# Optimization experiments

Measured on AMD Instinct MI355X. Metric: run time of the kernel, lower is better.

## Reference

```python
import jax, jax.numpy as jnp
import numpy as np

B, K, C, L = 16, 8, 64, 2048
OFFSET = 2.0  # self.offset in Coupling
EPS = 1e-7    # clamp for logit stability (flows' safe_log analogue)


def setup_inputs() -> dict:
    key = jax.random.key(0)
    ks = jax.random.split(key, 6)
    return {
        "x_change": jax.random.normal(ks[0], (B, C, L), jnp.float32),
        "a": jax.random.normal(ks[1], (B, C, L), jnp.float32),
        "b": jax.random.normal(ks[2], (B, C, L), jnp.float32),
        "pi": jax.random.normal(ks[3], (B, K, C, L), jnp.float32),
        "mu": jax.random.normal(ks[4], (B, K, C, L), jnp.float32),
        "s": jax.random.normal(ks[5], (B, K, C, L), jnp.float32) * 0.1,  # log-scales
        "sldj": jnp.zeros((B,), jnp.float32),
    }


def reference(x_change, a, b, pi, mu, s, sldj):
    # scale = sigmoid(a + offset) + (1 - sigmoid(offset))
    sig_off = 1.0 - jax.nn.sigmoid(jnp.float32(OFFSET))
    scale = jax.nn.sigmoid(a + OFFSET) + sig_off                      # [B,C,L]

    logpi = jax.nn.log_softmax(pi, axis=1)                            # [B,K,C,L]
    z = (x_change[:, None] - mu) * jnp.exp(-s)                        # [B,K,C,L]

    # logistic.mixture_log_cdf: logsumexp_k(log pi_k + log sigmoid(z_k))
    log_cdf = jax.scipy.special.logsumexp(logpi + jax.nn.log_sigmoid(z), axis=1)
    u = jnp.clip(jnp.exp(log_cdf), EPS, 1.0 - EPS)                    # [B,C,L]

    # logistic.inverse (forward): logit, with ldj = -log(u) - log(1-u)
    y = jnp.log(u) - jnp.log1p(-u)
    scale_ldj = -jnp.log(u) - jnp.log1p(-u)

    # logistic.mixture_log_pdf: logsumexp_k(log pi_k + z - s - 2 softplus(z))
    log_pdf = jax.scipy.special.logsumexp(
        logpi + z - s - 2.0 * jax.nn.softplus(z), axis=1)             # [B,C,L]

    sldj_out = sldj + jnp.sum(
        (log_pdf + scale_ldj + jnp.log(scale)).reshape(sldj.shape[0], -1), axis=-1)
    out = (y + b) * scale                                             # [B,C,L]
    return out, sldj_out
```

## Files before the change

kernel.cpp:

```cpp
#include <hip/hip_runtime.h>

#define BB 16
#define KK 8
#define CC 64
#define LL 2048

constexpr int CL = CC * LL;
constexpr int QUADS_PER_BATCH = CL / 4;
constexpr int NBLOCKS = (BB * QUADS_PER_BATCH) / 256;

#define SIG_OFF 0.11920292202211755f
#define LOG_EPS -16.11809565095832f

#define DEPTH 4

typedef float f32x4 __attribute__((ext_vector_type(4)));

__device__ __forceinline__ float frcp(float x) { return __builtin_amdgcn_rcpf(x); }

__device__ __forceinline__ f32x4 ds_read128(uint32_t addr) {
    f32x4 r;
    asm volatile("ds_read_b128 %0, %1" : "=v"(r) : "v"(addr));
    return r;
}

__device__ __forceinline__ void glds16(const float* gsrc, const float* ldst) {
    __builtin_amdgcn_global_load_lds(
        (const __attribute__((address_space(1))) void*)gsrc,
        (__attribute__((address_space(3))) void*)ldst,
        16, 0, 0);
}

__global__ void init_sldj_kernel(const float* __restrict__ sldj_in,
                                 float* __restrict__ sldj_out) {
    int i = threadIdx.x;
    if (i < BB) sldj_out[i] = sldj_in[i];
}

__global__ __launch_bounds__(256) void coupling_kernel(
    const float* __restrict__ x,
    const float* __restrict__ a,
    const float* __restrict__ bv,
    const float* __restrict__ pi,
    const float* __restrict__ mu,
    const float* __restrict__ s,
    float* __restrict__ out,
    float* __restrict__ sldj_out) {

    __shared__ __align__(16) float lds[DEPTH][3][1024];

    const int tid = threadIdx.x;
    const int idx = blockIdx.x * 256 + tid;
    const int b   = idx >> 15;
    const int rem = idx & (QUADS_PER_BATCH - 1);
    const int base = b * CL + rem * 4;
    const int wid  = tid >> 6;

    const f32x4 x4 = *(const f32x4*)(x + base);
    const f32x4 a4 = *(const f32x4*)(a + base);
    const f32x4 b4 = *(const f32x4*)(bv + base);
    __builtin_amdgcn_sched_barrier(0);

    const int kb0 = (b * KK) * CL + rem * 4;
    const float* pik = pi + kb0;
    const float* muk = mu + kb0;
    const float* svk = s  + kb0;

#pragma unroll
    for (int k = 0; k < DEPTH; ++k) {
        glds16(pik + k * CL, &lds[k][0][wid * 256]);
        glds16(muk + k * CL, &lds[k][1][wid * 256]);
        glds16(svk + k * CL, &lds[k][2][wid * 256]);
    }
    __builtin_amdgcn_sched_barrier(0);

    auto* l3 = (__attribute__((address_space(3))) float*)&lds[0][0][0];
    const uint32_t lds0 = (uint32_t)(size_t)l3 + (uint32_t)tid * 16u;

    float Spi[4] = {0.f, 0.f, 0.f, 0.f};
    float Nc[4]  = {0.f, 0.f, 0.f, 0.f};
    float N1[4]  = {0.f, 0.f, 0.f, 0.f};
    float Np[4]  = {0.f, 0.f, 0.f, 0.f};

#pragma unroll
    for (int k = 0; k < KK; ++k) {
        const int slot = k & (DEPTH - 1);

        if (k <= 4)      asm volatile("s_waitcnt vmcnt(9)" ::: "memory");
        else if (k == 5) asm volatile("s_waitcnt vmcnt(6)" ::: "memory");
        else if (k == 6) asm volatile("s_waitcnt vmcnt(3)" ::: "memory");
        else             asm volatile("s_waitcnt vmcnt(0)" ::: "memory");

        const uint32_t sa = lds0 + (uint32_t)(slot * 12288);
        f32x4 p4 = ds_read128(sa);
        f32x4 m4 = ds_read128(sa + 4096u);
        f32x4 s4 = ds_read128(sa + 8192u);

        asm volatile("s_waitcnt lgkmcnt(0)" ::: "memory");
        __builtin_amdgcn_sched_barrier(0);

        if (k < KK - DEPTH) {
            glds16(pik + (k + DEPTH) * CL, &lds[slot][0][wid * 256]);
            glds16(muk + (k + DEPTH) * CL, &lds[slot][1][wid * 256]);
            glds16(svk + (k + DEPTH) * CL, &lds[slot][2][wid * 256]);
        }

#pragma unroll
        for (int e = 0; e < 4; ++e) {
            const float p      = p4[e];
            const float m      = m4[e];
            const float sk     = s4[e];
            const float invstd = __expf(-sk);
            const float z      = (x4[e] - m) * invstd;

            const float t  = __expf(-fabsf(z));
            const float r  = frcp(1.f + t);
            const float tr = t * r;
            const float sig  = (z >= 0.f) ? r  : tr;
            const float osig = (z >= 0.f) ? tr : r;

            const float ek = __expf(p);
            Spi[e] += ek;
            Nc[e]  += ek * sig;
            N1[e]  += ek * osig;
            Np[e]  += ek * invstd * sig * osig;
        }
    }

    float contrib = 0.f;
    f32x4 out4;

#pragma unroll
    for (int e = 0; e < 4; ++e) {
        const float lSpi = __logf(Spi[e]);
        const float lu   = fmaxf(__logf(Nc[e]) - lSpi, LOG_EPS);
        const float lomu = fmaxf(__logf(N1[e]) - lSpi, LOG_EPS);
        const float y        = lu - lomu;
        const float ldj_term = -lu - lomu;
        const float log_pdf  = __logf(Np[e]) - lSpi;

        const float ae = a4[e] + 2.f;
        const float t2 = __expf(-fabsf(ae));
        const float r2 = frcp(1.f + t2);
        const float sc = ((ae >= 0.f) ? r2 : t2 * r2) + SIG_OFF;

        out4[e] = (y + b4[e]) * sc;
        contrib += log_pdf + ldj_term + __logf(sc);
    }

    *(f32x4*)(out + base) = out4;

#pragma unroll
    for (int off = 32; off > 0; off >>= 1)
        contrib += __shfl_down(contrib, off, 64);

    __shared__ float wsum[4];
    const int lane = tid & 63;
    if (lane == 0) wsum[wid] = contrib;
    __syncthreads();
    if (tid == 0) {
        atomicAdd(&sldj_out[b], wsum[0] + wsum[1] + wsum[2] + wsum[3]);
    }
}

extern "C" void kernel_launch(void* const* d_in, const int* in_sizes, int n_in,
                              void* d_out, int out_size, void* d_ws, size_t ws_size,
                              hipStream_t stream) {
    const float* x    = (const float*)d_in[0];
    const float* a    = (const float*)d_in[1];
    const float* bv   = (const float*)d_in[2];
    const float* pi   = (const float*)d_in[3];
    const float* mu   = (const float*)d_in[4];
    const float* s    = (const float*)d_in[5];
    const float* sldj = (const float*)d_in[6];

    float* out      = (float*)d_out;
    float* sldj_out = out + (size_t)BB * CL;

    init_sldj_kernel<<<1, 64, 0, stream>>>(sldj, sldj_out);
    coupling_kernel<<<NBLOCKS, 256, 0, stream>>>(x, a, bv, pi, mu, s, out, sldj_out);
}
```

Before: 224.3 us.

## Split mixture components across half-waves with direct register loads instead of LDS pipeline

Each wave now covers 32 quads, and the two half-waves each handle 4 of the 8 mixture components. The partial sums are combined with a cross-half shuffle, and only the lower half writes the output. The LDS staging through global_load_lds, with its manual vmcnt-gated ring buffer, is replaced by issuing all 12 vector loads straight into registers, with occupancy hinted by launch bounds. This frees LDS and doubles the thread count per element to raise memory-level parallelism, at the cost of twice as many blocks, redundant x/a/b loads and duplicated epilogue math.

New measurement: 224.8 us. Within noise of the previous version (+0.2%).

```diff
diff --git a/kernel.cpp b/kernel.cpp
--- a/kernel.cpp
+++ b/kernel.cpp
@@ -7,29 +7,14 @@
 
 constexpr int CL = CC * LL;
 constexpr int QUADS_PER_BATCH = CL / 4;
-constexpr int NBLOCKS = (BB * QUADS_PER_BATCH) / 256;
+constexpr int NBLOCKS = (BB * QUADS_PER_BATCH) / 128;
 
 #define SIG_OFF 0.11920292202211755f
 #define LOG_EPS -16.11809565095832f
 
-#define DEPTH 4
-
 typedef float f32x4 __attribute__((ext_vector_type(4)));
 
 __device__ __forceinline__ float frcp(float x) { return __builtin_amdgcn_rcpf(x); }
-
-__device__ __forceinline__ f32x4 ds_read128(uint32_t addr) {
-    f32x4 r;
-    asm volatile("ds_read_b128 %0, %1" : "=v"(r) : "v"(addr));
-    return r;
-}
-
-__device__ __forceinline__ void glds16(const float* gsrc, const float* ldst) {
-    __builtin_amdgcn_global_load_lds(
-        (const __attribute__((address_space(1))) void*)gsrc,
-        (__attribute__((address_space(3))) void*)ldst,
-        16, 0, 0);
-}
 
 __global__ void init_sldj_kernel(const float* __restrict__ sldj_in,
                                  float* __restrict__ sldj_out) {
@@ -37,7 +22,7 @@
     if (i < BB) sldj_out[i] = sldj_in[i];
 }
 
-__global__ __launch_bounds__(256) void coupling_kernel(
+__global__ __launch_bounds__(256, 4) void coupling_kernel(
     const float* __restrict__ x,
     const float* __restrict__ a,
     const float* __restrict__ bv,
@@ -47,35 +32,28 @@
     float* __restrict__ out,
     float* __restrict__ sldj_out) {
 
-    __shared__ __align__(16) float lds[DEPTH][3][1024];
-
-    const int tid = threadIdx.x;
-    const int idx = blockIdx.x * 256 + tid;
-    const int b   = idx >> 15;
-    const int rem = idx & (QUADS_PER_BATCH - 1);
-    const int base = b * CL + rem * 4;
+    const int tid  = threadIdx.x;
+    const int lane = tid & 63;
     const int wid  = tid >> 6;
+    const int kh   = lane >> 5;
+    const int q    = blockIdx.x * 128 + wid * 32 + (lane & 31);
+    const int b    = q >> 15;
+    const int base = q * 4;
+    const int rem4 = base - b * CL;
 
     const f32x4 x4 = *(const f32x4*)(x + base);
+
+    const int kb0 = (b * KK + kh * 4) * CL + rem4;
+    f32x4 pi4[4], mu4[4], s4[4];
+#pragma unroll
+    for (int j = 0; j < 4; ++j) {
+        pi4[j] = *(const f32x4*)(pi + kb0 + j * CL);
+        mu4[j] = *(const f32x4*)(mu + kb0 + j * CL);
+        s4[j]  = *(const f32x4*)(s  + kb0 + j * CL);
+    }
     const f32x4 a4 = *(const f32x4*)(a + base);
     const f32x4 b4 = *(const f32x4*)(bv + base);
     __builtin_amdgcn_sched_barrier(0);
-
-    const int kb0 = (b * KK) * CL + rem * 4;
-    const float* pik = pi + kb0;
-    const float* muk = mu + kb0;
-    const float* svk = s  + kb0;
-
-#pragma unroll
-    for (int k = 0; k < DEPTH; ++k) {
-        glds16(pik + k * CL, &lds[k][0][wid * 256]);
-        glds16(muk + k * CL, &lds[k][1][wid * 256]);
-        glds16(svk + k * CL, &lds[k][2][wid * 256]);
-    }
-    __builtin_amdgcn_sched_barrier(0);
-
-    auto* l3 = (__attribute__((address_space(3))) float*)&lds[0][0][0];
-    const uint32_t lds0 = (uint32_t)(size_t)l3 + (uint32_t)tid * 16u;
 
     float Spi[4] = {0.f, 0.f, 0.f, 0.f};
     float Nc[4]  = {0.f, 0.f, 0.f, 0.f};
@@ -83,33 +61,12 @@
     float Np[4]  = {0.f, 0.f, 0.f, 0.f};
 
 #pragma unroll
-    for (int k = 0; k < KK; ++k) {
-        const int slot = k & (DEPTH - 1);
-
-        if (k <= 4)      asm volatile("s_waitcnt vmcnt(9)" ::: "memory");
-        else if (k == 5) asm volatile("s_waitcnt vmcnt(6)" ::: "memory");
-        else if (k == 6) asm volatile("s_waitcnt vmcnt(3)" ::: "memory");
-        else             asm volatile("s_waitcnt vmcnt(0)" ::: "memory");
-
-        const uint32_t sa = lds0 + (uint32_t)(slot * 12288);
-        f32x4 p4 = ds_read128(sa);
-        f32x4 m4 = ds_read128(sa + 4096u);
-        f32x4 s4 = ds_read128(sa + 8192u);
-
-        asm volatile("s_waitcnt lgkmcnt(0)" ::: "memory");
-        __builtin_amdgcn_sched_barrier(0);
-
-        if (k < KK - DEPTH) {
-            glds16(pik + (k + DEPTH) * CL, &lds[slot][0][wid * 256]);
-            glds16(muk + (k + DEPTH) * CL, &lds[slot][1][wid * 256]);
-            glds16(svk + (k + DEPTH) * CL, &lds[slot][2][wid * 256]);
-        }
-
+    for (int j = 0; j < 4; ++j) {
 #pragma unroll
         for (int e = 0; e < 4; ++e) {
-            const float p      = p4[e];
-            const float m      = m4[e];
-            const float sk     = s4[e];
+            const float p      = pi4[j][e];
+            const float m      = mu4[j][e];
+            const float sk     = s4[j][e];
             const float invstd = __expf(-sk);
             const float z      = (x4[e] - m) * invstd;
 
@@ -125,6 +82,14 @@
             N1[e]  += ek * osig;
             Np[e]  += ek * invstd * sig * osig;
         }
+    }
+
+#pragma unroll
+    for (int e = 0; e < 4; ++e) {
+        Spi[e] += __shfl_xor(Spi[e], 32, 64);
+        Nc[e]  += __shfl_xor(Nc[e],  32, 64);
+        N1[e]  += __shfl_xor(N1[e],  32, 64);
+        Np[e]  += __shfl_xor(Np[e],  32, 64);
     }
 
     float contrib = 0.f;
@@ -148,14 +113,17 @@
         contrib += log_pdf + ldj_term + __logf(sc);
     }
 
-    *(f32x4*)(out + base) = out4;
+    if (kh == 0) {
+        *(f32x4*)(out + base) = out4;
+    } else {
+        contrib = 0.f;
+    }
 
 #pragma unroll
     for (int off = 32; off > 0; off >>= 1)
         contrib += __shfl_down(contrib, off, 64);
 
     __shared__ float wsum[4];
-    const int lane = tid & 63;
     if (lane == 0) wsum[wid] = contrib;
     __syncthreads();
     if (tid == 0) {
```
